# Kernel tuning notes

Hardware: AMD Instinct MI355X
Metric: run time of the kernel (lower is better)

## Reference

```python
import jax, jax.numpy as jnp
import numpy as np

NUM_Q_HEADS = 64
NUM_KV_HEADS = 8
HEAD_DIM = 64
HIDDEN = 2880
SLIDING_WINDOW = 128
ROPE_WAVELENGTH = 10000.0
NEG_INF = jnp.float32(-1e9)


def _rope(x, start_index=0):
    # x: (b, s, n, h). yarn with scaling_factor=1.0 == standard RoPE (split-half rotate).
    s, h = x.shape[1], x.shape[-1]
    inv_freq = 1.0 / (ROPE_WAVELENGTH ** (jnp.arange(0, h, 2, dtype=jnp.float32) / h))
    pos = jnp.arange(s, dtype=jnp.float32) + start_index
    freqs = pos[:, None] * inv_freq[None, :]  # (s, h/2)
    cos = jnp.concatenate([jnp.cos(freqs), jnp.cos(freqs)], axis=-1)[None, :, None, :]
    sin = jnp.concatenate([jnp.sin(freqs), jnp.sin(freqs)], axis=-1)[None, :, None, :]
    x1, x2 = jnp.split(x, 2, axis=-1)
    rot = jnp.concatenate([-x2, x1], axis=-1)
    return x * cos + rot * sin


def setup_inputs() -> dict:
    key = jax.random.key(0)
    ks = jax.random.split(key, 9)
    b, s = 1, 2048
    scale = 0.02
    hidden_states = jax.random.normal(ks[0], (b, s, HIDDEN), jnp.float32)
    Wq = jax.random.normal(ks[1], (HIDDEN, NUM_Q_HEADS, HEAD_DIM), jnp.float32) * scale
    Wk = jax.random.normal(ks[2], (HIDDEN, NUM_KV_HEADS, HEAD_DIM), jnp.float32) * scale
    Wv = jax.random.normal(ks[3], (HIDDEN, NUM_KV_HEADS, HEAD_DIM), jnp.float32) * scale
    Wo = jax.random.normal(ks[4], (NUM_Q_HEADS, HEAD_DIM, HIDDEN), jnp.float32) * scale
    bq = jnp.zeros((NUM_Q_HEADS, HEAD_DIM), jnp.float32)
    bk = jnp.zeros((NUM_KV_HEADS, HEAD_DIM), jnp.float32)
    bv = jnp.zeros((NUM_KV_HEADS, HEAD_DIM), jnp.float32)
    bo = jnp.zeros((HIDDEN,), jnp.float32)
    sinks = jax.random.normal(ks[5], (NUM_Q_HEADS,), jnp.float32) * 0.05
    attention_mask = jnp.tril(jnp.ones((s, s), bool))[None]  # causal, (b, q, k)
    return dict(hidden_states=hidden_states, Wq=Wq, bq=bq, Wk=Wk, bk=bk, Wv=Wv,
                bv=bv, Wo=Wo, bo=bo, sinks=sinks, attention_mask=attention_mask)


def reference(hidden_states, Wq, bq, Wk, bk, Wv, bv, Wo, bo, sinks, attention_mask):
    b, s, _ = hidden_states.shape
    inv_norm = 1.0 / np.sqrt(HEAD_DIM).astype(np.float32)
    # QKV projections (EinsumDense with bias)
    q = jnp.einsum('bqm,muh->bquh', hidden_states, Wq) + bq
    k = jnp.einsum('bkm,mvh->bkvh', hidden_states, Wk) + bk
    v = jnp.einsum('bkm,mvh->bkvh', hidden_states, Wv) + bv
    # rotary_dim == head_dim (even), so RoPE applies to the full head dim
    q = _rope(q)
    k = _rope(k)
    # GQA: repeat kv heads
    groups = NUM_Q_HEADS // NUM_KV_HEADS
    k = jnp.repeat(k, groups, axis=2)
    v = jnp.repeat(v, groups, axis=2)
    scores = jnp.einsum('bquh,bkuh->buqk', q, k) * inv_norm
    # sliding-window mask: keep kv_pos >= q_pos - window
    qpos = jnp.arange(s)
    swin = qpos[None, :] >= qpos[:, None] - SLIDING_WINDOW  # (q, k)
    scores = jnp.where(swin[None, None], scores, NEG_INF)
    scores = jnp.where(attention_mask[:, None], scores, NEG_INF)
    # sink-token logit per head appended as extra kv column
    sink = jnp.broadcast_to(sinks.reshape(1, NUM_Q_HEADS, 1, 1), (b, NUM_Q_HEADS, s, 1))
    logits = jnp.concatenate([scores, sink], axis=-1)
    m = jax.lax.stop_gradient(jnp.max(logits, axis=-1, keepdims=True))
    probs = jax.nn.softmax(logits - m, axis=-1)[..., :-1]  # drop sink column
    attn = jnp.einsum('buqk,bkuh->bquh', probs, v)
    return jnp.einsum('bquh,uhm->bqm', attn, Wo) + bo
```

## Files before the change

### kernel.cpp

```cpp
#include <hip/hip_runtime.h>
#include <cstdint>

typedef __attribute__((ext_vector_type(4))) float f32x4;
typedef __attribute__((ext_vector_type(8))) short bf16x8;

#define HIDDEN 2880
#define SEQ 2048
#define QKV_N 5120
#define WIN 128

__device__ __forceinline__ ushort f2bf(float f) {
  uint32_t u = __builtin_bit_cast(uint32_t, f);
  u += 0x7fff + ((u >> 16) & 1);
  return (ushort)(u >> 16);
}
__device__ __forceinline__ float bf2f(ushort h) {
  uint32_t u = ((uint32_t)h) << 16;
  return __builtin_bit_cast(float, u);
}

__global__ void conv_kernel(const float* __restrict__ in, ushort* __restrict__ out, int n) {
  int i = (blockIdx.x * blockDim.x + threadIdx.x) * 4;
  if (i >= n) return;
  float4 v = *(const float4*)(in + i);
  ushort4 o;
  o.x = f2bf(v.x); o.y = f2bf(v.y); o.z = f2bf(v.z); o.w = f2bf(v.w);
  *(ushort4*)(out + i) = o;
}

__global__ __launch_bounds__(256) void tconv_kernel(const float* __restrict__ in, ushort* __restrict__ out,
                                                    int R, int C, int out_ld, int out_row_off) {
  __shared__ float tile[32][33];
  int c0 = blockIdx.x * 32, r0 = blockIdx.y * 32;
  int tx = threadIdx.x & 31, ty = threadIdx.x >> 5;
#pragma unroll
  for (int i = 0; i < 32; i += 8)
    tile[ty + i][tx] = in[(size_t)(r0 + ty + i) * C + c0 + tx];
  __syncthreads();
#pragma unroll
  for (int i = 0; i < 32; i += 8)
    out[(size_t)(out_row_off + c0 + ty + i) * out_ld + r0 + tx] = f2bf(tile[tx][ty + i]);
}

__global__ void biascat_kernel(const float* __restrict__ bq, const float* __restrict__ bk,
                               const float* __restrict__ bv, float* __restrict__ out) {
  int i = blockIdx.x * blockDim.x + threadIdx.x;
  if (i >= QKV_N) return;
  float v = (i < 4096) ? bq[i] : (i < 4608) ? bk[i - 4096] : bv[i - 4608];
  out[i] = v;
}

__global__ void ropetab_kernel(float2* __restrict__ tab) {
  int i = blockIdx.x * blockDim.x + threadIdx.x;
  int s = i >> 5, d = i & 31;
  float inv = powf(10000.0f, -(float)d / 32.0f);
  float f = (float)s * inv;
  tab[i] = make_float2(cosf(f), sinf(f));
}

__global__ __launch_bounds__(256) void vt_kernel(const ushort* __restrict__ qkv, ushort* __restrict__ vt) {
  __shared__ ushort tile[64][80];
  int kv0 = blockIdx.x * 64, d0 = blockIdx.y * 64;
  int t = threadIdx.x;
#pragma unroll
  for (int p = 0; p < 2; ++p) {
    int lr = p * 32 + (t >> 3);
    *(bf16x8*)&tile[lr][(t & 7) * 8] =
        *(const bf16x8*)&qkv[(size_t)(kv0 + lr) * QKV_N + 4608 + d0 + (t & 7) * 8];
  }
  __syncthreads();
#pragma unroll
  for (int p = 0; p < 2; ++p) {
    int dl = p * 32 + (t >> 3);
    bf16x8 o;
#pragma unroll
    for (int jj = 0; jj < 8; ++jj) o[jj] = (short)tile[(t & 7) * 8 + jj][dl];
    *(bf16x8*)&vt[(size_t)(d0 + dl) * 2048 + kv0 + (t & 7) * 8] = o;
  }
}

template <int BN, bool OUT_BF16, bool ROPE>
__global__ __launch_bounds__(256, 2) void gemm4w_kernel(
    const ushort* __restrict__ A, const ushort* __restrict__ Bt,
    const float* __restrict__ bias, const float2* __restrict__ tab,
    void* __restrict__ Cv, int K, int lda, int ldb, int ldc) {
  constexpr int NFRAG = BN / 32;
  constexpr int BHALF = BN * 64;
  constexpr int BCHUNKS = BHALF / 1024;
  constexpr int BUFBYTES = 16384 + 2 * BHALF;
  static_assert(!ROPE || NFRAG == 4, "RoPE fusion requires BN=128");
  __shared__ __align__(16) char ldsbuf[2 * BUFBYTES];

  const int cpx = gridDim.x >> 3;
  const int wg = ((int)blockIdx.x & 7) * cpx + ((int)blockIdx.x >> 3);
  const int mtile = wg & 15, ntile = wg >> 4;
  const int m0 = mtile * 128, n0 = ntile * BN;

  const int tid = threadIdx.x, wv = tid >> 6, l = tid & 63;
  const int wm = wv >> 1, wn = wv & 1;
  const int r = l & 15, g = l >> 4;

  const int c = l ^ ((l >> 3) & 3);
  const ushort* gA0 = A + (size_t)(m0 + (c >> 2)) * lda + (c & 3) * 8;
  const ushort* gB0 = Bt + (size_t)(n0 + (c >> 2)) * ldb + (c & 3) * 8;

  const int gsw = (g * 16) ^ (((r >> 1) & 3) << 4);
  const int aOff = (wm * 64 + r) * 64 + gsw;
  const int bOff = (wn * (NFRAG * 16) + r) * 64 + gsw;

  auto sA = [&](int nb, int kg, int kh) {
#pragma unroll
    for (int j = 0; j < 2; ++j) {
      int cid = j * 4 + wv;
      __builtin_amdgcn_global_load_lds(
          (const __attribute__((address_space(1))) void*)(const void*)(gA0 + (size_t)cid * 16 * lda + kg),
          (__attribute__((address_space(3))) void*)&ldsbuf[nb * BUFBYTES + kh * 8192 + cid * 1024], 16, 0, 0);
    }
  };
  auto sB = [&](int nb, int kg, int kh) {
#pragma unroll
    for (int j = 0; j < (BCHUNKS + 3) / 4; ++j) {
      int cid = j * 4 + wv;
      if (cid < BCHUNKS)
        __builtin_amdgcn_global_load_lds(
            (const __attribute__((address_space(1))) void*)(const void*)(gB0 + (size_t)cid * 16 * ldb + kg),
            (__attribute__((address_space(3))) void*)&ldsbuf[nb * BUFBYTES + 16384 + kh * BHALF + cid * 1024],
            16, 0, 0);
    }
  };

#define BAR() __builtin_amdgcn_s_barrier()
#define LGKM0()                                              \
  do {                                                       \
    asm volatile("s_waitcnt lgkmcnt(0)" ::: "memory");       \
    __builtin_amdgcn_sched_barrier(0);                       \
  } while (0)
#define WAITV0() asm volatile("s_waitcnt vmcnt(0)" ::: "memory")

  f32x4 acc[4][NFRAG] = {};
  const int nt = K >> 6;

  sA(0, 0, 0); sA(0, 32, 1); sB(0, 0, 0); sB(0, 32, 1);
  WAITV0();
  BAR();

  for (int t = 0; t < nt; ++t) {
    const int bufOff = (t & 1) * BUFBYTES;
    const int nb = (t & 1) ^ 1;
    if (t + 1 < nt) {
      const int kn = (t + 1) * 64;
      sA(nb, kn, 0); sA(nb, kn + 32, 1);
      sB(nb, kn, 0); sB(nb, kn + 32, 1);
    }
#pragma unroll
    for (int kh = 0; kh < 2; ++kh) {
      bf16x8 aq[4], bq[NFRAG];
#pragma unroll
      for (int nf = 0; nf < NFRAG; ++nf)
        bq[nf] = *(const bf16x8*)&ldsbuf[bufOff + 16384 + kh * BHALF + bOff + nf * 1024];
#pragma unroll
      for (int mi = 0; mi < 4; ++mi)
        aq[mi] = *(const bf16x8*)&ldsbuf[bufOff + kh * 8192 + aOff + mi * 1024];
      LGKM0();
      __builtin_amdgcn_s_setprio(1);
#pragma unroll
      for (int mi = 0; mi < 4; ++mi)
#pragma unroll
        for (int nf = 0; nf < NFRAG; ++nf)
          acc[mi][nf] = __builtin_amdgcn_mfma_f32_16x16x32_bf16(aq[mi], bq[nf], acc[mi][nf], 0, 0, 0);
      __builtin_amdgcn_s_setprio(0);
    }
    WAITV0();
    BAR();
  }

  const bool doRope = ROPE && (n0 < 4608);
#pragma unroll
  for (int mf2 = 0; mf2 < 4; ++mf2) {
    float vb[NFRAG][4];
#pragma unroll
    for (int nf = 0; nf < NFRAG; ++nf) {
      int cc = n0 + wn * (NFRAG * 16) + nf * 16 + r;
      float b = bias[cc];
#pragma unroll
      for (int j = 0; j < 4; ++j) vb[nf][j] = acc[mf2][nf][j] + b;
    }
    if constexpr (ROPE) {
      if (doRope) {
#pragma unroll
        for (int j = 0; j < 4; ++j) {
          int s = m0 + wm * 64 + mf2 * 16 + g * 4 + j;
          float2 cs0 = tab[(s << 5) + r];
          float2 cs1 = tab[(s << 5) + 16 + r];
          float q0 = vb[0][j] * cs0.x - vb[2][j] * cs0.y;
          float q1 = vb[1][j] * cs1.x - vb[3][j] * cs1.y;
          float q2 = vb[2][j] * cs0.x + vb[0][j] * cs0.y;
          float q3 = vb[3][j] * cs1.x + vb[1][j] * cs1.y;
          vb[0][j] = q0; vb[1][j] = q1; vb[2][j] = q2; vb[3][j] = q3;
        }
      }
    }
#pragma unroll
    for (int nf = 0; nf < NFRAG; ++nf) {
      int cc = n0 + wn * (NFRAG * 16) + nf * 16 + r;
#pragma unroll
      for (int j = 0; j < 4; ++j) {
        int rrow = m0 + wm * 64 + mf2 * 16 + g * 4 + j;
        if (OUT_BF16) ((ushort*)Cv)[(size_t)rrow * ldc + cc] = f2bf(vb[nf][j]);
        else ((float*)Cv)[(size_t)rrow * ldc + cc] = vb[nf][j];
      }
    }
  }
#undef BAR
#undef LGKM0
#undef WAITV0
}

__global__ __launch_bounds__(512, 4) void attn_kernel(
    const ushort* __restrict__ qkv, const ushort* __restrict__ vt,
    const float* __restrict__ sinks, ushort* __restrict__ out) {
  __shared__ __align__(16) char lds[54272];
  const int kh = blockIdx.y;
  const int q0 = blockIdx.x * 32;
  const int kvw0 = q0 - 128;
  const int tid = threadIdx.x, w = tid >> 6, l = tid & 63;
  const int r = l & 15, g = l >> 4;
  const int h = kh * 8 + w;

  if (tid < 256) ((uint32_t*)(lds + 40960))[tid] = 0;

#pragma unroll
  for (int it = 0; it < 3; ++it) {
    int c = it * 512 + tid;
    if (c < 1280) {
      {
        int row = c >> 3, ch = c & 7;
        int kv = kvw0 + row;
        bf16x8 vv = {};
        if (kv >= 0) vv = *(const bf16x8*)&qkv[(size_t)kv * QKV_N + 4096 + kh * 64 + ch * 8];
        int byte = (row * 128 + ch * 16) ^ ((row & 7) << 4);
        *(bf16x8*)(lds + byte) = vv;
      }
      {
        int row = c / 20, ch = c - (c / 20) * 20;
        int kv = kvw0 + ch * 8;
        bf16x8 vv = {};
        if (kv >= 0) vv = *(const bf16x8*)&vt[(size_t)(kh * 64 + row) * 2048 + kv];
        int byte = (row * 320 + ch * 16) ^ ((row & 7) << 4);
        *(bf16x8*)(lds + 20480 + byte) = vv;
      }
    }
  }
  __syncthreads();

  char* Pw = lds + 41984 + w * 1536;
  const float snk = sinks[h];

#pragma unroll
  for (int si = 0; si < 2; ++si) {
    const ushort* qb = &qkv[(size_t)(q0 + si * 16 + r) * QKV_N + h * 64 + g * 8];
    bf16x8 qf0 = *(const bf16x8*)qb;
    bf16x8 qf1 = *(const bf16x8*)(qb + 32);

    f32x4 S[9];
    float mx[4] = {-3e30f, -3e30f, -3e30f, -3e30f};
#pragma unroll
    for (int tt = 0; tt < 9; ++tt) {
      int kvloc = (si + tt) * 16 + r;
      int b0 = (kvloc * 128 + g * 16) ^ ((kvloc & 7) << 4);
      int b1 = (kvloc * 128 + 64 + g * 16) ^ ((kvloc & 7) << 4);
      bf16x8 kf0 = *(const bf16x8*)(lds + b0);
      bf16x8 kf1 = *(const bf16x8*)(lds + b1);
      f32x4 s = {};
      s = __builtin_amdgcn_mfma_f32_16x16x32_bf16(qf0, kf0, s, 0, 0, 0);
      s = __builtin_amdgcn_mfma_f32_16x16x32_bf16(qf1, kf1, s, 0, 0, 0);
      int kvc = kvw0 + kvloc;
#pragma unroll
      for (int j = 0; j < 4; ++j) {
        int qr = q0 + si * 16 + g * 4 + j;
        bool valid = (kvc >= 0) && (kvc <= qr) && (kvc >= qr - WIN);
        float v = valid ? s[j] * 0.125f : -1e30f;
        s[j] = v;
        mx[j] = fmaxf(mx[j], v);
      }
      S[tt] = s;
    }
#pragma unroll
    for (int off = 1; off < 16; off <<= 1)
#pragma unroll
      for (int j = 0; j < 4; ++j) mx[j] = fmaxf(mx[j], __shfl_xor(mx[j], off, 64));
    float m[4], sum[4] = {0, 0, 0, 0};
#pragma unroll
    for (int j = 0; j < 4; ++j) m[j] = fmaxf(mx[j], snk);
#pragma unroll
    for (int tt = 0; tt < 9; ++tt)
#pragma unroll
      for (int j = 0; j < 4; ++j) {
        float p = (S[tt][j] > -1e29f) ? __expf(S[tt][j] - m[j]) : 0.0f;
        S[tt][j] = p;
        sum[j] += p;
      }
#pragma unroll
    for (int off = 1; off < 16; off <<= 1)
#pragma unroll
      for (int j = 0; j < 4; ++j) sum[j] += __shfl_xor(sum[j], off, 64);
    float rinv[4];
#pragma unroll
    for (int j = 0; j < 4; ++j) rinv[j] = 1.0f / (sum[j] + __expf(snk - m[j]));

    f32x4 acc[4] = {};
#pragma unroll
    for (int ks = 0; ks < 5; ++ks) {
#pragma unroll
      for (int c2 = 0; c2 < 2; ++c2) {
        int tt = 2 * ks + c2;
#pragma unroll
        for (int j = 0; j < 4; ++j) {
          float pv = (tt <= 8) ? S[tt][j] * rinv[j] : 0.0f;
          *(ushort*)(Pw + ((g * 4 + j) * 48 + c2 * 16 + r) * 2) = f2bf(pv);
        }
      }
      bf16x8 pa = *(const bf16x8*)(Pw + (r * 48 + g * 8) * 2);
#pragma unroll
      for (int ni = 0; ni < 4; ++ni) {
        int row = ni * 16 + r;
        int byte = (row * 320 + (si * 16 + ks * 32 + g * 8) * 2) ^ ((row & 7) << 4);
        bf16x8 vb = *(const bf16x8*)(lds + 20480 + byte);
        acc[ni] = __builtin_amdgcn_mfma_f32_16x16x32_bf16(pa, vb, acc[ni], 0, 0, 0);
      }
    }
#pragma unroll
    for (int ni = 0; ni < 4; ++ni)
#pragma unroll
      for (int j = 0; j < 4; ++j)
        out[(size_t)(q0 + si * 16 + g * 4 + j) * 4096 + h * 64 + ni * 16 + r] = f2bf(acc[ni][j]);
  }
}

extern "C" void kernel_launch(void* const* d_in, const int* in_sizes, int n_in,
                              void* d_out, int out_size, void* d_ws, size_t ws_size,
                              hipStream_t stream) {
  const float* hs = (const float*)d_in[0];
  const float* Wq = (const float*)d_in[1];
  const float* bq = (const float*)d_in[2];
  const float* Wk = (const float*)d_in[3];
  const float* bk = (const float*)d_in[4];
  const float* Wv = (const float*)d_in[5];
  const float* bv = (const float*)d_in[6];
  const float* Wo = (const float*)d_in[7];
  const float* bo = (const float*)d_in[8];
  const float* sinks = (const float*)d_in[9];
  float* out = (float*)d_out;

  char* ws = (char*)d_ws;
  ushort* hs_bf   = (ushort*)(ws + 0);
  ushort* vt_g    = (ushort*)(ws + 0);
  ushort* wqkv_t  = (ushort*)(ws + 11796480);
  ushort* attn    = (ushort*)(ws + 11796480);
  ushort* wo_t    = (ushort*)(ws + 41287680);
  ushort* qkv     = (ushort*)(ws + 66453504);
  float*  bias_all= (float*)(ws + 87425024);
  float2* tab     = (float2*)(ws + 87445504);

  conv_kernel<<<5898240 / 4 / 256, 256, 0, stream>>>(hs, hs_bf, 5898240);
  tconv_kernel<<<dim3(4096 / 32, 2880 / 32), 256, 0, stream>>>(Wq, wqkv_t, 2880, 4096, 2880, 0);
  tconv_kernel<<<dim3(512 / 32, 2880 / 32), 256, 0, stream>>>(Wk, wqkv_t, 2880, 512, 2880, 4096);
  tconv_kernel<<<dim3(512 / 32, 2880 / 32), 256, 0, stream>>>(Wv, wqkv_t, 2880, 512, 2880, 4608);
  tconv_kernel<<<dim3(2880 / 32, 4096 / 32), 256, 0, stream>>>(Wo, wo_t, 4096, 2880, 4096, 0);
  biascat_kernel<<<20, 256, 0, stream>>>(bq, bk, bv, bias_all);
  ropetab_kernel<<<2048 * 32 / 256, 256, 0, stream>>>(tab);

  gemm4w_kernel<128, true, true><<<640, 256, 0, stream>>>(hs_bf, wqkv_t, bias_all, tab, qkv,
                                                          2880, 2880, 2880, 5120);
  vt_kernel<<<dim3(32, 8), 256, 0, stream>>>(qkv, vt_g);
  attn_kernel<<<dim3(64, 8), 512, 0, stream>>>(qkv, vt_g, sinks, attn);
  gemm4w_kernel<160, false, false><<<288, 256, 0, stream>>>(attn, wo_t, bo, tab, out,
                                                            4096, 4096, 4096, 2880);
}
```

Baseline: 226.7 us.

## Widen conversion kernels, unfuse RoPE from QKV GEMM and retile with BN=160

Vectorizes the fp32→bf16 conversion to 8 elements per thread. Replaces the 32x32 weight-transpose kernel with a 64x64 tile version that converts to bf16 before staging in LDS and writes 16-byte rows. Removes the RoPE epilogue from the QKV GEMM, which lets the GEMM use BN=160 with 512 workgroups instead of 640, and adds a separate rope8 kernel that rotates Q and K in place in bf16. The extra pass over Q/K costs memory traffic and rounds twice to bf16, which slightly changes numerics.

```diff
diff --git a/kernel.cpp b/kernel.cpp
--- a/kernel.cpp
+++ b/kernel.cpp
@@ -20,26 +20,40 @@
 }
 
 __global__ void conv_kernel(const float* __restrict__ in, ushort* __restrict__ out, int n) {
-  int i = (blockIdx.x * blockDim.x + threadIdx.x) * 4;
+  int i = (blockIdx.x * blockDim.x + threadIdx.x) * 8;
   if (i >= n) return;
-  float4 v = *(const float4*)(in + i);
-  ushort4 o;
-  o.x = f2bf(v.x); o.y = f2bf(v.y); o.z = f2bf(v.z); o.w = f2bf(v.w);
-  *(ushort4*)(out + i) = o;
-}
-
-__global__ __launch_bounds__(256) void tconv_kernel(const float* __restrict__ in, ushort* __restrict__ out,
-                                                    int R, int C, int out_ld, int out_row_off) {
-  __shared__ float tile[32][33];
-  int c0 = blockIdx.x * 32, r0 = blockIdx.y * 32;
-  int tx = threadIdx.x & 31, ty = threadIdx.x >> 5;
-#pragma unroll
-  for (int i = 0; i < 32; i += 8)
-    tile[ty + i][tx] = in[(size_t)(r0 + ty + i) * C + c0 + tx];
+  float4 a = *(const float4*)(in + i);
+  float4 b = *(const float4*)(in + i + 4);
+  bf16x8 o;
+  o[0] = (short)f2bf(a.x); o[1] = (short)f2bf(a.y); o[2] = (short)f2bf(a.z); o[3] = (short)f2bf(a.w);
+  o[4] = (short)f2bf(b.x); o[5] = (short)f2bf(b.y); o[6] = (short)f2bf(b.z); o[7] = (short)f2bf(b.w);
+  *(bf16x8*)(out + i) = o;
+}
+
+__global__ __launch_bounds__(256) void tconv2_kernel(const float* __restrict__ in, ushort* __restrict__ out,
+                                                     int C, int out_ld, int out_row_off) {
+  __shared__ ushort tile[64][68];
+  int c0 = blockIdx.x * 64, r0 = blockIdx.y * 64;
+  int t = threadIdx.x;
+  int lr = t >> 4;
+  int lc = (t & 15) * 4;
+#pragma unroll
+  for (int i = 0; i < 4; ++i) {
+    float4 v = *(const float4*)&in[(size_t)(r0 + i * 16 + lr) * C + c0 + lc];
+    ushort4 o;
+    o.x = f2bf(v.x); o.y = f2bf(v.y); o.z = f2bf(v.z); o.w = f2bf(v.w);
+    *(ushort4*)&tile[i * 16 + lr][lc] = o;
+  }
   __syncthreads();
-#pragma unroll
-  for (int i = 0; i < 32; i += 8)
-    out[(size_t)(out_row_off + c0 + ty + i) * out_ld + r0 + tx] = f2bf(tile[tx][ty + i]);
+  int rr0 = (t & 7) * 8;
+#pragma unroll
+  for (int i2 = 0; i2 < 2; ++i2) {
+    int cc = i2 * 32 + (t >> 3);
+    bf16x8 o;
+#pragma unroll
+    for (int j = 0; j < 8; ++j) o[j] = (short)tile[rr0 + j][cc];
+    *(bf16x8*)&out[(size_t)(out_row_off + c0 + cc) * out_ld + r0 + rr0] = o;
+  }
 }
 
 __global__ void biascat_kernel(const float* __restrict__ bq, const float* __restrict__ bk,
@@ -58,6 +72,28 @@
   tab[i] = make_float2(cosf(f), sinf(f));
 }
 
+__global__ void rope8_kernel(ushort* __restrict__ buf, const float2* __restrict__ tab,
+                             int perrow , int total) {
+  int idx = blockIdx.x * blockDim.x + threadIdx.x;
+  if (idx >= total) return;
+  int s = idx / perrow;
+  int p = idx - s * perrow;
+  int head = p >> 2, j = p & 3;
+  ushort* base = buf + (size_t)s * QKV_N + head * 64 + j * 8;
+  bf16x8 x1 = *(const bf16x8*)base;
+  bf16x8 x2 = *(const bf16x8*)(base + 32);
+  bf16x8 o1, o2;
+#pragma unroll
+  for (int i = 0; i < 8; ++i) {
+    float2 cs = tab[(s << 5) + j * 8 + i];
+    float a = bf2f((ushort)x1[i]), b = bf2f((ushort)x2[i]);
+    o1[i] = (short)f2bf(a * cs.x - b * cs.y);
+    o2[i] = (short)f2bf(b * cs.x + a * cs.y);
+  }
+  *(bf16x8*)base = o1;
+  *(bf16x8*)(base + 32) = o2;
+}
+
 __global__ __launch_bounds__(256) void vt_kernel(const ushort* __restrict__ qkv, ushort* __restrict__ vt) {
   __shared__ ushort tile[64][80];
   int kv0 = blockIdx.x * 64, d0 = blockIdx.y * 64;
@@ -79,16 +115,15 @@
   }
 }
 
-template <int BN, bool OUT_BF16, bool ROPE>
+template <int BN, bool OUT_BF16>
 __global__ __launch_bounds__(256, 2) void gemm4w_kernel(
     const ushort* __restrict__ A, const ushort* __restrict__ Bt,
-    const float* __restrict__ bias, const float2* __restrict__ tab,
-    void* __restrict__ Cv, int K, int lda, int ldb, int ldc) {
+    const float* __restrict__ bias, void* __restrict__ Cv,
+    int K, int lda, int ldb, int ldc) {
   constexpr int NFRAG = BN / 32;
   constexpr int BHALF = BN * 64;
   constexpr int BCHUNKS = BHALF / 1024;
   constexpr int BUFBYTES = 16384 + 2 * BHALF;
-  static_assert(!ROPE || NFRAG == 4, "RoPE fusion requires BN=128");
   __shared__ __align__(16) char ldsbuf[2 * BUFBYTES];
 
   const int cpx = gridDim.x >> 3;
@@ -174,40 +209,18 @@
     BAR();
   }
 
-  const bool doRope = ROPE && (n0 < 4608);
 #pragma unroll
   for (int mf2 = 0; mf2 < 4; ++mf2) {
-    float vb[NFRAG][4];
 #pragma unroll
     for (int nf = 0; nf < NFRAG; ++nf) {
       int cc = n0 + wn * (NFRAG * 16) + nf * 16 + r;
       float b = bias[cc];
 #pragma unroll
-      for (int j = 0; j < 4; ++j) vb[nf][j] = acc[mf2][nf][j] + b;
-    }
-    if constexpr (ROPE) {
-      if (doRope) {
-#pragma unroll
-        for (int j = 0; j < 4; ++j) {
-          int s = m0 + wm * 64 + mf2 * 16 + g * 4 + j;
-          float2 cs0 = tab[(s << 5) + r];
-          float2 cs1 = tab[(s << 5) + 16 + r];
-          float q0 = vb[0][j] * cs0.x - vb[2][j] * cs0.y;
-          float q1 = vb[1][j] * cs1.x - vb[3][j] * cs1.y;
-          float q2 = vb[2][j] * cs0.x + vb[0][j] * cs0.y;
-          float q3 = vb[3][j] * cs1.x + vb[1][j] * cs1.y;
-          vb[0][j] = q0; vb[1][j] = q1; vb[2][j] = q2; vb[3][j] = q3;
-        }
-      }
-    }
-#pragma unroll
-    for (int nf = 0; nf < NFRAG; ++nf) {
-      int cc = n0 + wn * (NFRAG * 16) + nf * 16 + r;
-#pragma unroll
       for (int j = 0; j < 4; ++j) {
         int rrow = m0 + wm * 64 + mf2 * 16 + g * 4 + j;
-        if (OUT_BF16) ((ushort*)Cv)[(size_t)rrow * ldc + cc] = f2bf(vb[nf][j]);
-        else ((float*)Cv)[(size_t)rrow * ldc + cc] = vb[nf][j];
+        float v = acc[mf2][nf][j] + b;
+        if (OUT_BF16) ((ushort*)Cv)[(size_t)rrow * ldc + cc] = f2bf(v);
+        else ((float*)Cv)[(size_t)rrow * ldc + cc] = v;
       }
     }
   }
@@ -362,18 +375,20 @@
   float*  bias_all= (float*)(ws + 87425024);
   float2* tab     = (float2*)(ws + 87445504);
 
-  conv_kernel<<<5898240 / 4 / 256, 256, 0, stream>>>(hs, hs_bf, 5898240);
-  tconv_kernel<<<dim3(4096 / 32, 2880 / 32), 256, 0, stream>>>(Wq, wqkv_t, 2880, 4096, 2880, 0);
-  tconv_kernel<<<dim3(512 / 32, 2880 / 32), 256, 0, stream>>>(Wk, wqkv_t, 2880, 512, 2880, 4096);
-  tconv_kernel<<<dim3(512 / 32, 2880 / 32), 256, 0, stream>>>(Wv, wqkv_t, 2880, 512, 2880, 4608);
-  tconv_kernel<<<dim3(2880 / 32, 4096 / 32), 256, 0, stream>>>(Wo, wo_t, 4096, 2880, 4096, 0);
+  conv_kernel<<<5898240 / 8 / 256, 256, 0, stream>>>(hs, hs_bf, 5898240);
+  tconv2_kernel<<<dim3(64, 45), 256, 0, stream>>>(Wq, wqkv_t, 4096, 2880, 0);
+  tconv2_kernel<<<dim3(8, 45), 256, 0, stream>>>(Wk, wqkv_t, 512, 2880, 4096);
+  tconv2_kernel<<<dim3(8, 45), 256, 0, stream>>>(Wv, wqkv_t, 512, 2880, 4608);
+  tconv2_kernel<<<dim3(45, 64), 256, 0, stream>>>(Wo, wo_t, 2880, 4096, 0);
   biascat_kernel<<<20, 256, 0, stream>>>(bq, bk, bv, bias_all);
   ropetab_kernel<<<2048 * 32 / 256, 256, 0, stream>>>(tab);
 
-  gemm4w_kernel<128, true, true><<<640, 256, 0, stream>>>(hs_bf, wqkv_t, bias_all, tab, qkv,
-                                                          2880, 2880, 2880, 5120);
+  gemm4w_kernel<160, true><<<512, 256, 0, stream>>>(hs_bf, wqkv_t, bias_all, qkv,
+                                                    2880, 2880, 2880, 5120);
+  rope8_kernel<<<2048, 256, 0, stream>>>(qkv, tab, 256, 2048 * 256);
+  rope8_kernel<<<256, 256, 0, stream>>>(qkv + 4096, tab, 32, 2048 * 32);
   vt_kernel<<<dim3(32, 8), 256, 0, stream>>>(qkv, vt_g);
   attn_kernel<<<dim3(64, 8), 512, 0, stream>>>(qkv, vt_g, sinks, attn);
-  gemm4w_kernel<160, false, false><<<288, 256, 0, stream>>>(attn, wo_t, bo, tab, out,
-                                                            4096, 4096, 4096, 2880);
-}
+  gemm4w_kernel<160, false><<<288, 256, 0, stream>>>(attn, wo_t, bo, out,
+                                                     4096, 4096, 4096, 2880);
+}
```

After: 208.6 us. -8.0%, faster.
